# Optimization experiments

Hardware: AMD Instinct MI355X
Metric: run time of the kernel (lower is better)

The kernel has to match this reference:

```python
import itertools
import jax, jax.numpy as jnp
import numpy as np

ORDER = 3  # MaskDE(order=3) -> DescartesExtension orders 2..3
D = 80
B = 8192


def setup_inputs() -> dict:
    key = jax.random.key(0)
    kx, km = jax.random.split(key)
    x = jax.random.normal(kx, (B, D), dtype=jnp.float32)
    mask = jax.random.randint(km, (D,), 0, 2).astype(jnp.bool_)
    return {"x": x, "mask": mask}


def _comb_indices(m: int, order: int) -> np.ndarray:
    # combinations with replacement of range(m), shape (n_comb, order)
    return np.array(list(itertools.combinations_with_replacement(range(m), order)), dtype=np.int32)


def reference(x, mask):
    # mask is a concrete bool vector: masked_select == static gather
    idx = np.flatnonzero(np.asarray(mask))  # (m,)
    m = idx.size
    xm = x[:, idx]  # (B, m)
    parts = [xm]
    for order in range(2, ORDER + 1):
        combs = _comb_indices(m, order)           # (C, order)
        # gather-multiply-reduce: prod of each feature combination
        parts.append(jnp.prod(xm[:, combs], axis=-1))  # (B, C)
    return jnp.concatenate(parts, axis=-1)
```

## Files before the change

### kernel.cpp

```cpp
#include <hip/hip_runtime.h>
#include <stdint.h>

#define DMAX 80
#define BLK  256

typedef float f32x4 __attribute__((ext_vector_type(4)));

__global__ void maskde_setup(const void* __restrict__ mask_raw, int m,
                             int* __restrict__ idx_out,
                             uint32_t* __restrict__ pairtab,
                             uint32_t* __restrict__ coltab, int P) {
    int tid = blockIdx.x * blockDim.x + threadIdx.x;
    if (tid == 0) {
        const uint8_t* b8  = (const uint8_t*)mask_raw;
        const int*     b32 = (const int*)mask_raw;
        const float*   bf  = (const float*)mask_raw;
        int cnt = 0; bool ok = true;
        for (int i = 0; i < DMAX; ++i) { uint8_t v = b8[i]; if (v > 1) ok = false; cnt += (v != 0); }
        int mode;
        if (ok && cnt == m) {
            mode = 0;
        } else {
            cnt = 0; ok = true;
            for (int i = 0; i < DMAX; ++i) { int v = b32[i]; if (v != 0 && v != 1) ok = false; cnt += (v != 0); }
            mode = (ok && cnt == m) ? 1 : 2;
        }
        int k = 0;
        for (int i = 0; i < DMAX && k < m; ++i) {
            bool on = (mode == 0) ? (b8[i] != 0)
                    : (mode == 1) ? (b32[i] != 0)
                                  : (bf[i] != 0.0f);
            if (on) idx_out[k++] = i;
        }
    }

    int stride = gridDim.x * blockDim.x;
    for (int p = tid; p < P; p += stride) {
        int rem = p, i = 0;
        while (rem >= m - i) { rem -= (m - i); ++i; }
        int j = i + rem;

        pairtab[p] = (uint32_t)i | ((uint32_t)j << 8);

        if (p < m)
            coltab[p] = (uint32_t)P | ((uint32_t)p << 16);
        coltab[m + p] = (uint32_t)p | ((uint32_t)m << 16);

        int mi = m - i;
        long long Si  = ((long long)m * (m + 1) * (m + 2)
                       - (long long)mi * (mi + 1) * (mi + 2)) / 6;
        int Rij = ((m - i) + (m - j + 1)) * (j - i) / 2;
        uint32_t* t3 = coltab + m + P + Si + Rij;
        for (int k3 = j; k3 < m; ++k3)
            t3[k3 - j] = (uint32_t)p | ((uint32_t)k3 << 16);
    }
}

__global__ void maskde_copies(uint32_t* __restrict__ coltab, int tpad, int T,
                              int m, int P) {
    int q = blockIdx.x * blockDim.x + threadIdx.x;
    int total = 3 * tpad;
    uint32_t sentinel = (uint32_t)P | ((uint32_t)m << 16);
    for (; q < total; q += gridDim.x * blockDim.x) {
        int s   = 1 + q / tpad;
        int off = q - (s - 1) * tpad;
        uint32_t v = (off + s < T) ? coltab[off + s] : sentinel;
        coltab[s * tpad + off] = v;
    }
}

__global__ __launch_bounds__(BLK) void
maskde_expand(const float* __restrict__ x, const int* __restrict__ idx,
              const uint32_t* __restrict__ pairtab,
              const uint32_t* __restrict__ coltab, int tpad,
              float* __restrict__ out, int m, int T, int P) {
    __shared__ float xls[DMAX + 1];
    extern __shared__ float pps[];

    const int row = blockIdx.x;
    const int tid = threadIdx.x;

    if (tid <= m)
        xls[tid] = (tid < m) ? x[row * DMAX + idx[tid]] : 1.0f;
    __syncthreads();

    for (int p = tid; p <= P; p += BLK) {
        float v = 1.0f;
        if (p < P) {
            uint32_t ij = pairtab[p];
            v = xls[ij & 0xFF] * xls[(ij >> 8) & 0xFF];
        }
        pps[p] = v;
    }
    __syncthreads();

    float* orow = out + (size_t)row * (size_t)T;
    uintptr_t a0 = (uintptr_t)orow;
    int k0 = (int)(((16 - (a0 & 15)) & 15) >> 2);
    if (k0 > T) k0 = T;

    if (tid < k0) {
        uint32_t e = coltab[tid];
        orow[tid] = pps[e & 0xFFFF] * xls[e >> 16];
    }

    const int nv = (T - k0) >> 2;
    const uint4* tbv = (const uint4*)(coltab + (size_t)k0 * (size_t)tpad);
    float* ovbase = orow + k0;

    for (int v = tid; v < nv; v += BLK) {
        uint4 e = tbv[v];
        f32x4 o;
        o.x = pps[e.x & 0xFFFF] * xls[e.x >> 16];
        o.y = pps[e.y & 0xFFFF] * xls[e.y >> 16];
        o.z = pps[e.z & 0xFFFF] * xls[e.z >> 16];
        o.w = pps[e.w & 0xFFFF] * xls[e.w >> 16];
        *(f32x4*)(ovbase + 4 * v) = o;
    }

    int c = k0 + 4 * nv + tid;
    if (c < T) {
        uint32_t e = coltab[c];
        orow[c] = pps[e & 0xFFFF] * xls[e >> 16];
    }
}

extern "C" void kernel_launch(void* const* d_in, const int* in_sizes, int n_in,
                              void* d_out, int out_size, void* d_ws, size_t ws_size,
                              hipStream_t stream) {
    const float* x    = (const float*)d_in[0];
    const void*  mask = d_in[1];
    float*       out  = (float*)d_out;

    int rows = in_sizes[0] / DMAX;
    if (rows <= 0 || out_size <= 0) return;
    long long T = (long long)out_size / rows;

    int m = -1;
    for (int mm = 0; mm <= DMAX; ++mm) {
        long long t = (long long)mm
                    + (long long)mm * (mm + 1) / 2
                    + (long long)mm * (mm + 1) * (mm + 2) / 6;
        if (t == T) { m = mm; break; }
    }
    if (m <= 0) return;

    int P    = m * (m + 1) / 2;
    int tpad = (int)((T + 3) & ~3LL);

    int*      idx     = (int*)d_ws;
    uint32_t* pairtab = (uint32_t*)((char*)d_ws + 1024);
    uint32_t* coltab  = (uint32_t*)((char*)d_ws + 32768);

    int sblocks = (P + 255) / 256;
    if (sblocks < 1) sblocks = 1;
    maskde_setup<<<sblocks, 256, 0, stream>>>(mask, m, idx, pairtab, coltab, P);

    int cblocks = (3 * tpad + 255) / 256;
    maskde_copies<<<cblocks, 256, 0, stream>>>(coltab, tpad, (int)T, m, P);

    size_t shmem = (size_t)(P + 1) * sizeof(float);
    maskde_expand<<<rows, BLK, shmem, stream>>>(x, idx, pairtab, coltab, tpad,
                                                out, m, (int)T, P);
}
```

Baseline: 135.1 us.

## Fold shifted coltab copies into setup and map one wave per row

The separate maskde_copies kernel is removed. Setup now writes each coltab entry directly into all four shifted copies and fills the sentinel tail, which saves one launch and a read-back pass. The expand kernel now gives each 64-lane wave its own output row, four rows per block, each with private LDS for x values and pair products. Each row therefore gets a quarter of the threads it had before, so more blocks and rows can be resident at once. The risks are the serial sentinel fill in thread 0 and a per-row loop that is four times longer.

```diff
diff --git a/kernel.cpp b/kernel.cpp
--- a/kernel.cpp
+++ b/kernel.cpp
@@ -3,14 +3,18 @@
 
 #define DMAX 80
 #define BLK  256
+#define WPB  4
 
 typedef float f32x4 __attribute__((ext_vector_type(4)));
 
 __global__ void maskde_setup(const void* __restrict__ mask_raw, int m,
                              int* __restrict__ idx_out,
                              uint32_t* __restrict__ pairtab,
-                             uint32_t* __restrict__ coltab, int P) {
+                             uint32_t* __restrict__ coltab, int tpad, int T,
+                             int P) {
     int tid = blockIdx.x * blockDim.x + threadIdx.x;
+    uint32_t sentinel = (uint32_t)P | ((uint32_t)m << 16);
+
     if (tid == 0) {
         const uint8_t* b8  = (const uint8_t*)mask_raw;
         const int*     b32 = (const int*)mask_raw;
@@ -32,6 +36,9 @@
                                   : (bf[i] != 0.0f);
             if (on) idx_out[k++] = i;
         }
+        for (int s = 1; s <= 3; ++s)
+            for (int q = T - s; q < tpad; ++q)
+                if (q >= 0) coltab[s * tpad + q] = sentinel;
     }
 
     int stride = gridDim.x * blockDim.x;
@@ -42,30 +49,27 @@
 
         pairtab[p] = (uint32_t)i | ((uint32_t)j << 8);
 
+        #define WR4(c, v) do {                                             \
+            int _c = (c); uint32_t _v = (v);                               \
+            coltab[_c] = _v;                                               \
+            if (_c >= 1) coltab[tpad     + _c - 1] = _v;                   \
+            if (_c >= 2) coltab[2 * tpad + _c - 2] = _v;                   \
+            if (_c >= 3) coltab[3 * tpad + _c - 3] = _v;                   \
+        } while (0)
+
         if (p < m)
-            coltab[p] = (uint32_t)P | ((uint32_t)p << 16);
-        coltab[m + p] = (uint32_t)p | ((uint32_t)m << 16);
+            WR4(p, (uint32_t)P | ((uint32_t)p << 16));
+        WR4(m + p, (uint32_t)p | ((uint32_t)m << 16));
 
         int mi = m - i;
         long long Si  = ((long long)m * (m + 1) * (m + 2)
                        - (long long)mi * (mi + 1) * (mi + 2)) / 6;
         int Rij = ((m - i) + (m - j + 1)) * (j - i) / 2;
-        uint32_t* t3 = coltab + m + P + Si + Rij;
+        int base = m + P + (int)Si + Rij;
+        uint32_t pk = (uint32_t)p;
         for (int k3 = j; k3 < m; ++k3)
-            t3[k3 - j] = (uint32_t)p | ((uint32_t)k3 << 16);
-    }
-}
-
-__global__ void maskde_copies(uint32_t* __restrict__ coltab, int tpad, int T,
-                              int m, int P) {
-    int q = blockIdx.x * blockDim.x + threadIdx.x;
-    int total = 3 * tpad;
-    uint32_t sentinel = (uint32_t)P | ((uint32_t)m << 16);
-    for (; q < total; q += gridDim.x * blockDim.x) {
-        int s   = 1 + q / tpad;
-        int off = q - (s - 1) * tpad;
-        uint32_t v = (off + s < T) ? coltab[off + s] : sentinel;
-        coltab[s * tpad + off] = v;
+            WR4(base + (k3 - j), pk | ((uint32_t)k3 << 16));
+        #undef WR4
     }
 }
 
@@ -73,42 +77,51 @@
 maskde_expand(const float* __restrict__ x, const int* __restrict__ idx,
               const uint32_t* __restrict__ pairtab,
               const uint32_t* __restrict__ coltab, int tpad,
-              float* __restrict__ out, int m, int T, int P) {
-    __shared__ float xls[DMAX + 1];
-    extern __shared__ float pps[];
+              float* __restrict__ out, int m, int T, int P, int rows) {
+    extern __shared__ float smem[];
+    const int XSTR  = m + 1;
+    const int PPSTR = P + 1;
 
-    const int row = blockIdx.x;
-    const int tid = threadIdx.x;
+    const int wave = threadIdx.x >> 6;
+    const int lane = threadIdx.x & 63;
+    const int row  = blockIdx.x * WPB + wave;
+    const bool active = (row < rows);
 
-    if (tid <= m)
-        xls[tid] = (tid < m) ? x[row * DMAX + idx[tid]] : 1.0f;
+    float* xls = smem + wave * (XSTR + PPSTR);
+    float* pps = xls + XSTR;
+
+    if (active && lane <= m)
+        xls[lane] = (lane < m) ? x[row * DMAX + idx[lane]] : 1.0f;
     __syncthreads();
 
-    for (int p = tid; p <= P; p += BLK) {
-        float v = 1.0f;
-        if (p < P) {
-            uint32_t ij = pairtab[p];
-            v = xls[ij & 0xFF] * xls[(ij >> 8) & 0xFF];
+    if (active) {
+        for (int p = lane; p <= P; p += 64) {
+            float v = 1.0f;
+            if (p < P) {
+                uint32_t ij = pairtab[p];
+                v = xls[ij & 0xFF] * xls[(ij >> 8) & 0xFF];
+            }
+            pps[p] = v;
         }
-        pps[p] = v;
     }
     __syncthreads();
+    if (!active) return;
 
     float* orow = out + (size_t)row * (size_t)T;
     uintptr_t a0 = (uintptr_t)orow;
     int k0 = (int)(((16 - (a0 & 15)) & 15) >> 2);
     if (k0 > T) k0 = T;
 
-    if (tid < k0) {
-        uint32_t e = coltab[tid];
-        orow[tid] = pps[e & 0xFFFF] * xls[e >> 16];
+    if (lane < k0) {
+        uint32_t e = coltab[lane];
+        orow[lane] = pps[e & 0xFFFF] * xls[e >> 16];
     }
 
     const int nv = (T - k0) >> 2;
     const uint4* tbv = (const uint4*)(coltab + (size_t)k0 * (size_t)tpad);
     float* ovbase = orow + k0;
 
-    for (int v = tid; v < nv; v += BLK) {
+    for (int v = lane; v < nv; v += 64) {
         uint4 e = tbv[v];
         f32x4 o;
         o.x = pps[e.x & 0xFFFF] * xls[e.x >> 16];
@@ -118,7 +131,7 @@
         *(f32x4*)(ovbase + 4 * v) = o;
     }
 
-    int c = k0 + 4 * nv + tid;
+    int c = k0 + 4 * nv + lane;
     if (c < T) {
         uint32_t e = coltab[c];
         orow[c] = pps[e & 0xFFFF] * xls[e >> 16];
@@ -154,12 +167,11 @@
 
     int sblocks = (P + 255) / 256;
     if (sblocks < 1) sblocks = 1;
-    maskde_setup<<<sblocks, 256, 0, stream>>>(mask, m, idx, pairtab, coltab, P);
+    maskde_setup<<<sblocks, 256, 0, stream>>>(mask, m, idx, pairtab, coltab,
+                                              tpad, (int)T, P);
 
-    int cblocks = (3 * tpad + 255) / 256;
-    maskde_copies<<<cblocks, 256, 0, stream>>>(coltab, tpad, (int)T, m, P);
-
-    size_t shmem = (size_t)(P + 1) * sizeof(float);
-    maskde_expand<<<rows, BLK, shmem, stream>>>(x, idx, pairtab, coltab, tpad,
-                                                out, m, (int)T, P);
+    int blocks = (rows + WPB - 1) / WPB;
+    size_t shmem = (size_t)WPB * (size_t)(m + 1 + P + 1) * sizeof(float);
+    maskde_expand<<<blocks, BLK, shmem, stream>>>(x, idx, pairtab, coltab, tpad,
+                                                  out, m, (int)T, P, rows);
 }
```

New measurement: 147.5 us. +9.2%, slower.

## Stage column-table chunks in LDS and reuse them across groups of rows

Applied to the files above, without the earlier changes.

The expand kernel now splits output columns into chunks and loads each chunk of the index table into swizzled shared memory once per block. That chunk is reused across 16 rows, four waves each writing one row per pass, instead of every row re-reading the whole table from global memory. The alignment-shifted table copies and their separate kernel are dropped, and the pair table is shrunk to 16-bit entries. Costs are more shared memory per block, extra block-wide barriers per row group, and redundant pair-product work repeated in every column chunk.

```diff
diff --git a/kernel.cpp b/kernel.cpp
--- a/kernel.cpp
+++ b/kernel.cpp
@@ -3,14 +3,23 @@
 
 #define DMAX 80
 #define BLK  256
+#define WPB  4
+#define RPW  4
+#define RPB  (WPB * RPW)
+#define CW   3584
 
 typedef float f32x4 __attribute__((ext_vector_type(4)));
+
+__device__ __forceinline__ int swz(int q) { return q + (q >> 5); }
 
 __global__ void maskde_setup(const void* __restrict__ mask_raw, int m,
                              int* __restrict__ idx_out,
-                             uint32_t* __restrict__ pairtab,
-                             uint32_t* __restrict__ coltab, int P) {
+                             uint16_t* __restrict__ pair16,
+                             uint32_t* __restrict__ coltab,
+                             int T, int P, int padend) {
     int tid = blockIdx.x * blockDim.x + threadIdx.x;
+    uint32_t sentinel = (uint32_t)P | ((uint32_t)m << 16);
+
     if (tid == 0) {
         const uint8_t* b8  = (const uint8_t*)mask_raw;
         const int*     b32 = (const int*)mask_raw;
@@ -32,15 +41,19 @@
                                   : (bf[i] != 0.0f);
             if (on) idx_out[k++] = i;
         }
+        for (int q = -4; q < 0; ++q) coltab[q] = sentinel;
     }
 
     int stride = gridDim.x * blockDim.x;
+    for (int q = T + tid; q < padend; q += stride)
+        coltab[q] = sentinel;
+
     for (int p = tid; p < P; p += stride) {
         int rem = p, i = 0;
         while (rem >= m - i) { rem -= (m - i); ++i; }
         int j = i + rem;
 
-        pairtab[p] = (uint32_t)i | ((uint32_t)j << 8);
+        pair16[p] = (uint16_t)(i | (j << 8));
 
         if (p < m)
             coltab[p] = (uint32_t)P | ((uint32_t)p << 16);
@@ -50,78 +63,111 @@
         long long Si  = ((long long)m * (m + 1) * (m + 2)
                        - (long long)mi * (mi + 1) * (mi + 2)) / 6;
         int Rij = ((m - i) + (m - j + 1)) * (j - i) / 2;
-        uint32_t* t3 = coltab + m + P + Si + Rij;
+        int base = m + P + (int)Si + Rij;
         for (int k3 = j; k3 < m; ++k3)
-            t3[k3 - j] = (uint32_t)p | ((uint32_t)k3 << 16);
-    }
-}
-
-__global__ void maskde_copies(uint32_t* __restrict__ coltab, int tpad, int T,
-                              int m, int P) {
-    int q = blockIdx.x * blockDim.x + threadIdx.x;
-    int total = 3 * tpad;
-    uint32_t sentinel = (uint32_t)P | ((uint32_t)m << 16);
-    for (; q < total; q += gridDim.x * blockDim.x) {
-        int s   = 1 + q / tpad;
-        int off = q - (s - 1) * tpad;
-        uint32_t v = (off + s < T) ? coltab[off + s] : sentinel;
-        coltab[s * tpad + off] = v;
+            coltab[base + (k3 - j)] = (uint32_t)p | ((uint32_t)k3 << 16);
     }
 }
 
 __global__ __launch_bounds__(BLK) void
 maskde_expand(const float* __restrict__ x, const int* __restrict__ idx,
-              const uint32_t* __restrict__ pairtab,
-              const uint32_t* __restrict__ coltab, int tpad,
-              float* __restrict__ out, int m, int T, int P) {
-    __shared__ float xls[DMAX + 1];
-    extern __shared__ float pps[];
-
-    const int row = blockIdx.x;
-    const int tid = threadIdx.x;
-
-    if (tid <= m)
-        xls[tid] = (tid < m) ? x[row * DMAX + idx[tid]] : 1.0f;
+              const uint16_t* __restrict__ pair16g,
+              const uint32_t* __restrict__ coltab,
+              float* __restrict__ out,
+              int m, int T, int P, int rows, int nchunks) {
+    extern __shared__ uint8_t smraw[];
+    const int tabw  = swz(CW + 8) + 1;
+    uint32_t* tabL  = (uint32_t*)smraw;
+    uint16_t* pairL = (uint16_t*)(smraw + (size_t)tabw * 4);
+    float*    fbase = (float*)(smraw + (size_t)tabw * 4 + ((2 * P + 15) & ~15));
+    const int XSTR  = m + 1;
+    const int PPSTR = P + 1;
+
+    const int chunk = blockIdx.x % nchunks;
+    const int rowg  = blockIdx.x / nchunks;
+    const int c0    = chunk * CW;
+    const bool lastc = (chunk == nchunks - 1);
+    const int tid  = threadIdx.x;
+    const int wave = tid >> 6;
+    const int lane = tid & 63;
+
+    for (int q = tid; q < CW + 8; q += BLK)
+        tabL[swz(q)] = coltab[c0 - 4 + q];
+    for (int p = tid; p < P; p += BLK)
+        pairL[p] = pair16g[p];
     __syncthreads();
 
-    for (int p = tid; p <= P; p += BLK) {
-        float v = 1.0f;
-        if (p < P) {
-            uint32_t ij = pairtab[p];
-            v = xls[ij & 0xFF] * xls[(ij >> 8) & 0xFF];
-        }
-        pps[p] = v;
-    }
-    __syncthreads();
-
-    float* orow = out + (size_t)row * (size_t)T;
-    uintptr_t a0 = (uintptr_t)orow;
-    int k0 = (int)(((16 - (a0 & 15)) & 15) >> 2);
-    if (k0 > T) k0 = T;
-
-    if (tid < k0) {
-        uint32_t e = coltab[tid];
-        orow[tid] = pps[e & 0xFFFF] * xls[e >> 16];
-    }
-
-    const int nv = (T - k0) >> 2;
-    const uint4* tbv = (const uint4*)(coltab + (size_t)k0 * (size_t)tpad);
-    float* ovbase = orow + k0;
-
-    for (int v = tid; v < nv; v += BLK) {
-        uint4 e = tbv[v];
-        f32x4 o;
-        o.x = pps[e.x & 0xFFFF] * xls[e.x >> 16];
-        o.y = pps[e.y & 0xFFFF] * xls[e.y >> 16];
-        o.z = pps[e.z & 0xFFFF] * xls[e.z >> 16];
-        o.w = pps[e.w & 0xFFFF] * xls[e.w >> 16];
-        *(f32x4*)(ovbase + 4 * v) = o;
-    }
-
-    int c = k0 + 4 * nv + tid;
-    if (c < T) {
-        uint32_t e = coltab[c];
-        orow[c] = pps[e & 0xFFFF] * xls[e >> 16];
+    float* xls = fbase + wave * (XSTR + PPSTR);
+    float* pps = xls + XSTR;
+
+    for (int rr = 0; rr < RPW; ++rr) {
+        const int rowbase = rowg * RPB + rr * WPB;
+
+        for (int w = 0; w < WPB; ++w) {
+            int row = rowbase + w;
+            if (row < rows) {
+                float* xw = fbase + w * (XSTR + PPSTR);
+                for (int k = tid; k <= m; k += BLK)
+                    xw[k] = (k < m) ? x[row * DMAX + idx[k]] : 1.0f;
+            }
+        }
+        __syncthreads();
+
+        for (int w = 0; w < WPB; ++w) {
+            int row = rowbase + w;
+            if (row < rows) {
+                const float* xw = fbase + w * (XSTR + PPSTR);
+                float*       pw = (float*)(xw + XSTR);
+                for (int p = tid; p <= P; p += BLK) {
+                    float v = 1.0f;
+                    if (p < P) {
+                        uint32_t ij = pairL[p];
+                        v = xw[ij & 0xFF] * xw[(ij >> 8) & 0xFF];
+                    }
+                    pw[p] = v;
+                }
+            }
+        }
+        __syncthreads();
+
+        const int row = rowbase + wave;
+        if (row < rows) {
+            const long long rT = (long long)row * (long long)T;
+            float* orow = out + rT;
+            int a = (c0 == 0) ? 0 : c0 - (int)((rT + c0) & 3);
+            int b = lastc ? T : (c0 + CW - (int)((rT + c0 + CW) & 3));
+            int astart = a + (int)((4 - ((rT + a) & 3)) & 3);
+            if (astart > b) astart = b;
+
+            if (lane < astart - a) {
+                int c = a + lane;
+                uint32_t e = tabL[swz(c - c0 + 4)];
+                orow[c] = pps[e & 0xFFFF] * xls[e >> 16];
+            }
+
+            const int nvv = (b - astart) >> 2;
+            for (int v = lane; v < nvv; v += 64) {
+                int c  = astart + 4 * v;
+                int ib = c - c0 + 4;
+                uint32_t e0 = tabL[swz(ib)];
+                uint32_t e1 = tabL[swz(ib + 1)];
+                uint32_t e2 = tabL[swz(ib + 2)];
+                uint32_t e3 = tabL[swz(ib + 3)];
+                f32x4 o;
+                o.x = pps[e0 & 0xFFFF] * xls[e0 >> 16];
+                o.y = pps[e1 & 0xFFFF] * xls[e1 >> 16];
+                o.z = pps[e2 & 0xFFFF] * xls[e2 >> 16];
+                o.w = pps[e3 & 0xFFFF] * xls[e3 >> 16];
+                *(f32x4*)(orow + c) = o;
+            }
+
+            int c = astart + 4 * nvv + lane;
+            if (c < b) {
+                uint32_t e = tabL[swz(c - c0 + 4)];
+                orow[c] = pps[e & 0xFFFF] * xls[e >> 16];
+            }
+        }
+        __syncthreads();
     }
 }
 
@@ -145,21 +191,25 @@
     }
     if (m <= 0) return;
 
-    int P    = m * (m + 1) / 2;
-    int tpad = (int)((T + 3) & ~3LL);
-
-    int*      idx     = (int*)d_ws;
-    uint32_t* pairtab = (uint32_t*)((char*)d_ws + 1024);
-    uint32_t* coltab  = (uint32_t*)((char*)d_ws + 32768);
+    int P       = m * (m + 1) / 2;
+    int nchunks = (int)((T + CW - 1) / CW);
+    int padend  = nchunks * CW + 4;
+
+    int*      idx    = (int*)d_ws;
+    uint16_t* pair16 = (uint16_t*)((char*)d_ws + 1024);
+    uint32_t* coltab = (uint32_t*)((char*)d_ws + 32768) + 4;
 
     int sblocks = (P + 255) / 256;
     if (sblocks < 1) sblocks = 1;
-    maskde_setup<<<sblocks, 256, 0, stream>>>(mask, m, idx, pairtab, coltab, P);
-
-    int cblocks = (3 * tpad + 255) / 256;
-    maskde_copies<<<cblocks, 256, 0, stream>>>(coltab, tpad, (int)T, m, P);
-
-    size_t shmem = (size_t)(P + 1) * sizeof(float);
-    maskde_expand<<<rows, BLK, shmem, stream>>>(x, idx, pairtab, coltab, tpad,
-                                                out, m, (int)T, P);
+    maskde_setup<<<sblocks, 256, 0, stream>>>(mask, m, idx, pair16, coltab,
+                                              (int)T, P, padend);
+
+    int rowgroups = (rows + RPB - 1) / RPB;
+    int grid = rowgroups * nchunks;
+
+    int tabw = (CW + 8) + ((CW + 8) >> 5) + 1;
+    size_t shmem = (size_t)tabw * 4 + ((2 * P + 15) & ~15)
+                 + (size_t)WPB * (m + 1 + P + 1) * sizeof(float);
+    maskde_expand<<<grid, BLK, shmem, stream>>>(x, idx, pair16, coltab, out,
+                                                m, (int)T, P, rows, nchunks);
 }
```

After: 171.8 us. 1.27x slower.
